# Kernel optimization log

Measured on AMD Instinct MI355X. Metric: run time of the kernel, lower is better.

Reference implementation:

```python
import jax, jax.numpy as jnp
import numpy as np

H, CH, PQ, PV = 12, 16, 4, 8
C_S = 384
INF, EPS = 1e5, 1e-8
PT_W = -0.5


def setup_inputs() -> dict:
    key = jax.random.key(0)
    ks = jax.random.split(key, 20)
    B, C, N = 1, 8, 256
    s = jax.random.normal(ks[0], (B, C, N, C_S), jnp.float32)
    z = jax.random.normal(ks[1], (B, C, N, N, 8), jnp.float32)
    A = jax.random.normal(ks[2], (B, C, N, 3, 3), jnp.float32)
    rot = jnp.linalg.qr(A)[0]  # proper orthonormal frames
    trans = jax.random.normal(ks[3], (B, C, N, 3), jnp.float32) * 10.0
    mask = jnp.ones((B, C, N), jnp.float32)
    w = lambda k, i, o: jax.random.normal(k, (i, o), jnp.float32) * 0.02
    hc = H * CH
    return {
        's': s, 'z': z, 'rot': rot, 'trans': trans, 'mask': mask,
        'wq': w(ks[4], C_S, hc), 'bq': jnp.zeros((hc,)),
        'wkv': w(ks[5], C_S, 2 * hc), 'bkv': jnp.zeros((2 * hc,)),
        'g_gamma': jnp.ones((C_S,)), 'g_beta': jnp.zeros((C_S,)),
        'wgq': w(ks[6], C_S, hc), 'bgq': jnp.zeros((hc,)),
        'wgk': w(ks[7], C_S, hc), 'bgk': jnp.zeros((hc,)),
        'wqp': w(ks[8], C_S, H * PQ * 3), 'bqp': jnp.zeros((H * PQ * 3,)),
        'wkvp': w(ks[9], C_S, H * (PQ + PV) * 3), 'bkvp': jnp.zeros((H * (PQ + PV) * 3,)),
        'head_weights': jnp.full((H,), 0.5413248538970947, jnp.float32),  # softplus^-1(1)
        'wdist': w(ks[10], 1, H), 'bdist': jnp.zeros((H,)),
        'wout': w(ks[11], H * (CH + 4 * PV), C_S), 'bout': jnp.zeros((C_S,)),
    }


def _forward(s, z, rot, trans, mask, wq, bq, wkv, bkv, g_gamma, g_beta,
             wgq, bgq, wgk, bgk, wqp, bqp, wkvp, bkvp, head_weights,
             wdist, bdist, wout, bout):
    B, C, N, _ = s.shape
    q = (s @ wq + bq).reshape(B, C, N, H, CH)
    kv = (s @ wkv + bkv).reshape(B, C, N, H, 2 * CH)
    k, v = kv[..., :CH], kv[..., CH:]
    scale = (1.0 / (3 * CH)) ** 0.5
    a = jnp.einsum('bcihd,bcjhd->bchij', q, k) * scale  # [B,C,H,N,N]
    # global feature: mean over conformations, LayerNorm, QK bias
    s_g = s.mean(axis=-3)
    mu = s_g.mean(-1, keepdims=True)
    var = ((s_g - mu) ** 2).mean(-1, keepdims=True)
    s_gn = (s_g - mu) / jnp.sqrt(var + 1e-5) * g_gamma + g_beta
    g_q = (s_gn @ wgq + bgq).reshape(B, N, H, CH)
    g_k = (s_gn @ wgk + bgk).reshape(B, N, H, CH)
    a = a + jnp.einsum('bihd,bjhd->bhij', g_q, g_k)[:, None] * scale
    # invariant point attention term
    def to_pts(raw, P):
        pts = jnp.stack(jnp.split(raw, 3, axis=-1), axis=-1)  # [B,C,N,H*P,3]
        pts = jnp.einsum('bcnij,bcnpj->bcnpi', rot, pts) + trans[..., None, :]
        return pts.reshape(B, C, N, H, P, 3)
    q_pts = to_pts(s @ wqp + bqp, PQ)
    kv_pts = to_pts(s @ wkvp + bkvp, PQ + PV)
    k_pts, v_pts = kv_pts[..., :PQ, :], kv_pts[..., PQ:, :]
    diff2 = jnp.sum((q_pts[:, :, :, None] - k_pts[:, :, None]) ** 2, axis=-1)  # [B,C,N,N,H,PQ]
    hw = jax.nn.softplus(head_weights) * (1.0 / (3 * (PQ * 9.0 / 2))) ** 0.5
    pt_att = jnp.sum(diff2 * hw[:, None], axis=-1) * PT_W  # [B,C,N,N,H]
    a = a + jnp.moveaxis(pt_att, -1, -3)
    # mask
    sq_mask = mask[..., :, None] * mask[..., None, :]
    a = a + (INF * (sq_mask - 1.0))[..., None, :, :]
    # distance bias (torch uses a raw .view -> reshape, not transpose)
    dist = jnp.sqrt(jnp.sum((trans[..., :, None, :] - trans[..., None, :, :]) ** 2, axis=-1))
    db = dist[..., None] * wdist[0] + bdist  # [B,C,N,N,H]
    a = a + db.reshape(B, C, H, N, N)
    a = jax.nn.softmax(a, axis=-1)
    o = jnp.einsum('bchij,bcjhd->bcihd', a, v).reshape(B, C, N, H * CH)
    o_pt = jnp.einsum('bchij,bcjhpd->bcihpd', a, v_pts)  # [B,C,N,H,PV,3]
    o_pt = jnp.einsum('bcnji,bcnhpj->bcnhpi', rot, o_pt - trans[:, :, :, None, None, :])
    o_pt_norm = jnp.sqrt(jnp.sum(o_pt ** 2, axis=-1) + EPS).reshape(B, C, N, H * PV)
    o_pt_f = o_pt.reshape(B, C, N, H * PV, 3)
    feat = jnp.concatenate([o, o_pt_f[..., 0], o_pt_f[..., 1], o_pt_f[..., 2], o_pt_norm], axis=-1)
    return feat @ wout + bout, a


def reference(s, z, rot, trans, mask, wq, bq, wkv, bkv, g_gamma, g_beta,
              wgq, bgq, wgk, bgk, wqp, bqp, wkvp, bkvp, head_weights,
              wdist, bdist, wout, bout):
    return _forward(s, z, rot, trans, mask, wq, bq, wkv, bkv, g_gamma, g_beta,
                    wgq, bgq, wgk, bgk, wqp, bqp, wkvp, bkvp, head_weights,
                    wdist, bdist, wout, bout)
```

## Files before the change

### kernel.cpp

```cpp
#include <hip/hip_runtime.h>
#include <math.h>

#define NRES 256
#define CDIM 8
#define HNUM 12
#define CS   384

typedef __attribute__((ext_vector_type(8))) short bf16x8;
typedef __attribute__((ext_vector_type(4))) float f32x4;
typedef unsigned short ushort_t;

static __device__ __forceinline__ unsigned short f2bf(float x) {
    unsigned int u = __float_as_uint(x);
    unsigned int r = (u + 0x7fffu + ((u >> 16) & 1u)) >> 16;
    return (unsigned short)r;
}
static __device__ __forceinline__ float bf2f(unsigned short h) {
    return __uint_as_float(((unsigned int)h) << 16);
}

__global__ __launch_bounds__(256) void convert_kernel(
    const float* __restrict__ s,
    const float* __restrict__ wq, const float* __restrict__ bq,
    const float* __restrict__ wkv, const float* __restrict__ bkv,
    const float* __restrict__ wqp, const float* __restrict__ bqp,
    const float* __restrict__ wkvp, const float* __restrict__ bkvp,
    const float* __restrict__ wgq, const float* __restrict__ bgq,
    const float* __restrict__ wgk, const float* __restrict__ bgk,
    const float* __restrict__ wout,
    ushort_t* __restrict__ s_bf, ushort_t* __restrict__ wt_bf,
    ushort_t* __restrict__ wtg_bf, float* __restrict__ pbias,
    float* __restrict__ gbias,
    ushort_t* __restrict__ wo_hi, ushort_t* __restrict__ wo_lo)
{
    const int idx = blockIdx.x*256 + threadIdx.x;
    const int NS   = 2048*384;
    const int NWT  = 384*1152;
    const int NWTG = 384*384;
    const int NWO  = 576*384;
    if (idx < NS) {
        s_bf[idx] = f2bf(s[idx]);
    } else if (idx < NS + NWT) {
        const int t = idx - NS;
        const int k = t / 1152, vc = t - k*1152;
        const float* w; int C, lc;
        if (vc < 192)      { w = wq;   C = 192; lc = vc; }
        else if (vc < 576) { w = wkv;  C = 384; lc = vc - 192; }
        else if (vc < 720) { w = wqp;  C = 144; lc = vc - 576; }
        else               { w = wkvp; C = 432; lc = vc - 720; }
        wt_bf[(size_t)vc*384 + k] = f2bf(w[(size_t)k*C + lc]);
    } else if (idx < NS + NWT + NWTG) {
        const int t = idx - NS - NWT;
        const int k = t / 384, vc = t - k*384;
        const float val = (vc < 192) ? wgq[(size_t)k*192 + vc]
                                     : wgk[(size_t)k*192 + vc - 192];
        wtg_bf[(size_t)vc*384 + k] = f2bf(val);
    } else if (idx < NS + NWT + NWTG + 1152) {
        const int i = idx - NS - NWT - NWTG;
        float b;
        if (i < 192)      b = bq[i];
        else if (i < 576) b = bkv[i - 192];
        else if (i < 720) b = bqp[i - 576];
        else              b = bkvp[i - 720];
        pbias[i] = b;
    } else if (idx < NS + NWT + NWTG + 1152 + 384) {
        const int i = idx - NS - NWT - NWTG - 1152;
        gbias[i] = (i < 192) ? bgq[i] : bgk[i - 192];
    } else if (idx < NS + NWT + NWTG + 1536 + NWO) {
        const int t = idx - NS - NWT - NWTG - 1536;
        const int k = t / 384, n = t - k*384;
        const float wv = wout[t];
        const unsigned int u = __float_as_uint(wv);
        const float hif = __uint_as_float(u & 0xFFFF0000u);
        wo_hi[(size_t)n*576 + k] = (ushort_t)(u >> 16);
        wo_lo[(size_t)n*576 + k] = (ushort_t)(__float_as_uint(wv - hif) >> 16);
    }
}

__global__ __launch_bounds__(256) void proj_mfma_kernel(
    const ushort_t* __restrict__ s_bf, const ushort_t* __restrict__ wt_bf,
    const float* __restrict__ pbias,
    float* __restrict__ qo, float* __restrict__ ko, float* __restrict__ vo,
    float* __restrict__ rawp)
{
    const int blk = blockIdx.x;
    const int rt = blk / 18, ct = blk - rt*18;
    const int r0 = rt * 64, c0 = ct * 64;
    const int tid = threadIdx.x;
    const int wave = tid >> 6, lane = tid & 63;
    const int wrow = wave >> 1, wcol = wave & 1;
    const int m0 = r0 + wrow*32, n0 = c0 + wcol*32;
    const int qd = lane >> 4, lr = lane & 15;

    f32x4 acc00 = {0,0,0,0}, acc01 = {0,0,0,0}, acc10 = {0,0,0,0}, acc11 = {0,0,0,0};

    const ushort_t* a0p = s_bf  + (size_t)(m0 + lr)*384 + qd*8;
    const ushort_t* a1p = a0p + 16*384;
    const ushort_t* b0p = wt_bf + (size_t)(n0 + lr)*384 + qd*8;
    const ushort_t* b1p = b0p + 16*384;

    #pragma unroll
    for (int kk = 0; kk < 384; kk += 32) {
        const bf16x8 a0 = *(const bf16x8*)(a0p + kk);
        const bf16x8 a1 = *(const bf16x8*)(a1p + kk);
        const bf16x8 b0 = *(const bf16x8*)(b0p + kk);
        const bf16x8 b1 = *(const bf16x8*)(b1p + kk);
        acc00 = __builtin_amdgcn_mfma_f32_16x16x32_bf16(a0, b0, acc00, 0, 0, 0);
        acc01 = __builtin_amdgcn_mfma_f32_16x16x32_bf16(a0, b1, acc01, 0, 0, 0);
        acc10 = __builtin_amdgcn_mfma_f32_16x16x32_bf16(a1, b0, acc10, 0, 0, 0);
        acc11 = __builtin_amdgcn_mfma_f32_16x16x32_bf16(a1, b1, acc11, 0, 0, 0);
    }

    #pragma unroll
    for (int mt = 0; mt < 2; ++mt) {
        #pragma unroll
        for (int nt = 0; nt < 2; ++nt) {
            const f32x4 av = (mt==0) ? (nt==0 ? acc00 : acc01)
                                     : (nt==0 ? acc10 : acc11);
            const int col = n0 + nt*16 + lr;
            const float bb = pbias[col];
            #pragma unroll
            for (int reg = 0; reg < 4; ++reg) {
                const int row = m0 + mt*16 + qd*4 + reg;
                const float val = av[reg] + bb;
                if (col < 192) {
                    qo[(size_t)row*192 + col] = val;
                } else if (col < 576) {
                    const int lc = col - 192, h = lc >> 5, rm = lc & 31;
                    if (rm < 16) ko[(size_t)row*192 + h*16 + rm] = val;
                    else         vo[(size_t)row*192 + h*16 + rm - 16] = val;
                } else {
                    rawp[(size_t)row*576 + col - 576] = val;
                }
            }
        }
    }
}

__global__ __launch_bounds__(256) void pt_transform_kernel(
    const float* __restrict__ rawp, const float* __restrict__ rot,
    const float* __restrict__ trans,
    float* __restrict__ qpo, float* __restrict__ kpo, float* __restrict__ vpo)
{
    const int t = blockIdx.x*256 + threadIdx.x;
    const int row = t / 192;
    const int p = t - row*192;
    const float* R = rot + (size_t)row*9;
    const float* T = trans + (size_t)row*3;
    const float* base = rawp + (size_t)row*576;
    float x, y, z;
    if (p < 48) { x = base[p];       y = base[48+p];  z = base[96+p]; }
    else { const int pk = p-48; x = base[144+pk]; y = base[288+pk]; z = base[432+pk]; }
    const float px = R[0]*x + R[1]*y + R[2]*z + T[0];
    const float py = R[3]*x + R[4]*y + R[5]*z + T[1];
    const float pz = R[6]*x + R[7]*y + R[8]*z + T[2];
    if (p < 48) {
        float* o = qpo + (size_t)row*144 + p*3;
        o[0]=px; o[1]=py; o[2]=pz;
    } else {
        const int pk = p-48, h = pk/12, pp = pk - h*12;
        if (pp < 4) { float* o = kpo + (size_t)row*144 + (h*4+pp)*3;     o[0]=px; o[1]=py; o[2]=pz; }
        else        { float* o = vpo + (size_t)row*288 + (h*8+(pp-4))*3; o[0]=px; o[1]=py; o[2]=pz; }
    }
}

__global__ __launch_bounds__(256) void ln_kernel(
    const float* __restrict__ s, const float* __restrict__ g_gamma,
    const float* __restrict__ g_beta, ushort_t* __restrict__ sgn_bf)
{
    const int n = blockIdx.x;
    const int tid = threadIdx.x;
    __shared__ float sg[CS];
    __shared__ float red[256];

    for (int d = tid; d < CS; d += 256) {
        float acc = 0.f;
        for (int c = 0; c < CDIM; ++c) acc += s[((size_t)c*NRES+n)*CS + d];
        sg[d] = acc * (1.0f/CDIM);
    }
    __syncthreads();

    float lsum = 0.f;
    for (int d = tid; d < CS; d += 256) lsum += sg[d];
    red[tid] = lsum; __syncthreads();
    for (int st = 128; st > 0; st >>= 1) { if (tid < st) red[tid] += red[tid+st]; __syncthreads(); }
    const float mean = red[0] * (1.0f/CS);
    __syncthreads();

    float lvar = 0.f;
    for (int d = tid; d < CS; d += 256) { float df = sg[d]-mean; lvar += df*df; }
    red[tid] = lvar; __syncthreads();
    for (int st = 128; st > 0; st >>= 1) { if (tid < st) red[tid] += red[tid+st]; __syncthreads(); }
    const float var = red[0] * (1.0f/CS);
    __syncthreads();

    const float inv = rsqrtf(var + 1e-5f);
    for (int d = tid; d < CS; d += 256)
        sgn_bf[(size_t)n*CS + d] = f2bf((sg[d]-mean)*inv*g_gamma[d] + g_beta[d]);
}

__global__ __launch_bounds__(256) void ggemm_mfma_kernel(
    const ushort_t* __restrict__ sgn_bf, const ushort_t* __restrict__ wtg_bf,
    const float* __restrict__ gbias,
    float* __restrict__ gqo, float* __restrict__ gko)
{
    const int blk = blockIdx.x;
    const int rt = blk / 6, ct = blk - rt*6;
    const int r0 = rt * 64, c0 = ct * 64;
    const int tid = threadIdx.x;
    const int wave = tid >> 6, lane = tid & 63;
    const int wrow = wave >> 1, wcol = wave & 1;
    const int m0 = r0 + wrow*32, n0 = c0 + wcol*32;
    const int qd = lane >> 4, lr = lane & 15;

    f32x4 acc00 = {0,0,0,0}, acc01 = {0,0,0,0}, acc10 = {0,0,0,0}, acc11 = {0,0,0,0};

    const ushort_t* a0p = sgn_bf + (size_t)(m0 + lr)*384 + qd*8;
    const ushort_t* a1p = a0p + 16*384;
    const ushort_t* b0p = wtg_bf + (size_t)(n0 + lr)*384 + qd*8;
    const ushort_t* b1p = b0p + 16*384;

    #pragma unroll
    for (int kk = 0; kk < 384; kk += 32) {
        const bf16x8 a0 = *(const bf16x8*)(a0p + kk);
        const bf16x8 a1 = *(const bf16x8*)(a1p + kk);
        const bf16x8 b0 = *(const bf16x8*)(b0p + kk);
        const bf16x8 b1 = *(const bf16x8*)(b1p + kk);
        acc00 = __builtin_amdgcn_mfma_f32_16x16x32_bf16(a0, b0, acc00, 0, 0, 0);
        acc01 = __builtin_amdgcn_mfma_f32_16x16x32_bf16(a0, b1, acc01, 0, 0, 0);
        acc10 = __builtin_amdgcn_mfma_f32_16x16x32_bf16(a1, b0, acc10, 0, 0, 0);
        acc11 = __builtin_amdgcn_mfma_f32_16x16x32_bf16(a1, b1, acc11, 0, 0, 0);
    }

    #pragma unroll
    for (int mt = 0; mt < 2; ++mt) {
        #pragma unroll
        for (int nt = 0; nt < 2; ++nt) {
            const f32x4 av = (mt==0) ? (nt==0 ? acc00 : acc01)
                                     : (nt==0 ? acc10 : acc11);
            const int col = n0 + nt*16 + lr;
            const float bb = gbias[col];
            #pragma unroll
            for (int reg = 0; reg < 4; ++reg) {
                const int row = m0 + mt*16 + qd*4 + reg;
                const float val = av[reg] + bb;
                if (col < 192) gqo[(size_t)row*192 + col]       = val;
                else           gko[(size_t)row*192 + col - 192] = val;
            }
        }
    }
}

#define BSTR 104
__global__ __launch_bounds__(256) void attn_mfma_kernel(
    const float* __restrict__ q, const float* __restrict__ k,
    const float* __restrict__ q_pts, const float* __restrict__ k_pts,
    const float* __restrict__ g_q, const float* __restrict__ g_k,
    const float* __restrict__ trans, const float* __restrict__ mask,
    const float* __restrict__ head_weights, const float* __restrict__ wdist,
    const float* __restrict__ bdist, float* __restrict__ a_out)
{
    const int blk  = blockIdx.x;
    const int qtr  = blk & 3;
    const int ch   = blk >> 2;
    const int h    = ch % HNUM;
    const int c    = ch / HNUM;
    const int i0   = qtr * 64;
    const int tid  = threadIdx.x;

    __shared__ ushort_t Bsh[256*BSTR];
    __shared__ ushort_t Ash[64*BSTR];
    __shared__ float dsh[7*256];
    __shared__ float msh[256];
    __shared__ float kn_sh[256];
    __shared__ float qn_sh[64];
    __shared__ float wdsh[12], bdsh[12];
    __shared__ float cpart[96];
    __shared__ float censh[3];

    msh[tid] = mask[c*NRES + tid];
    if (tid < 12) { wdsh[tid] = wdist[tid]; bdsh[tid] = bdist[tid]; }

    if (tid < 96) {
        const int coord = tid % 3, chunk = tid / 3;
        float sv = 0.f;
        for (int e = 0; e < 8; ++e)
            sv += trans[((size_t)c*NRES + chunk*8 + e)*3 + coord];
        cpart[tid] = sv;
    }
    __syncthreads();
    if (tid < 3) {
        float sv = 0.f;
        for (int e = 0; e < 32; ++e) sv += cpart[e*3 + tid];
        censh[tid] = sv * (1.0f/256.0f);
    }
    __syncthreads();

    const float s54   = 0.13608276348795434f;
    const float scale = 0.14433756729740643f;
    const float hwv = 0.5f * logf(1.0f + expf(head_weights[h])) * s54;
    const float sh  = sqrtf(2.0f * hwv);
    const float cx = censh[0], cy = censh[1], cz = censh[2];
    const float cen3[3] = {cx, cy, cz};

    {
        const int j = tid;
        const float4* kr4 = (const float4*)(k    + ((size_t)c*NRES + j)*192 + h*16);
        const float4* gk4 = (const float4*)(g_k  + (size_t)j*192 + h*16);
        const float4* kp4 = (const float4*)(k_pts+ ((size_t)c*NRES + j)*144 + h*12);
        ushort_t* br = &Bsh[j*BSTR];
        #pragma unroll
        for (int e4 = 0; e4 < 4; ++e4) {
            const float4 w = kr4[e4];
            br[e4*4+0] = f2bf(w.x); br[e4*4+1] = f2bf(w.y);
            br[e4*4+2] = f2bf(w.z); br[e4*4+3] = f2bf(w.w);
        }
        #pragma unroll
        for (int e4 = 0; e4 < 4; ++e4) {
            const float4 w = gk4[e4];
            br[16+e4*4+0] = f2bf(w.x); br[16+e4*4+1] = f2bf(w.y);
            br[16+e4*4+2] = f2bf(w.z); br[16+e4*4+3] = f2bf(w.w);
        }
        float kp_a[12];
        #pragma unroll
        for (int e4 = 0; e4 < 3; ++e4) {
            const float4 w = kp4[e4];
            kp_a[e4*4+0]=w.x; kp_a[e4*4+1]=w.y; kp_a[e4*4+2]=w.z; kp_a[e4*4+3]=w.w;
        }
        float kn = 0.f;
        #pragma unroll
        for (int e = 0; e < 12; ++e) {
            const float kp = kp_a[e] - cen3[e % 3];
            kn += kp*kp;
            const float sp = sh * kp;
            const unsigned int u = __float_as_uint(sp);
            const float hif = __uint_as_float(u & 0xFFFF0000u);
            const ushort_t hi = (ushort_t)(u >> 16);
            br[32+e] = hi;
            br[44+e] = (ushort_t)(__float_as_uint(sp - hif) >> 16);
            br[56+e] = hi;
        }
        #pragma unroll
        for (int e = 68; e < 96; ++e) br[e] = 0;
        kn_sh[j] = hwv * kn;
    }

    if (tid < 64) {
        const int il = i0 + tid;
        const float4* qr4 = (const float4*)(q    + ((size_t)c*NRES + il)*192 + h*16);
        const float4* gq4 = (const float4*)(g_q  + (size_t)il*192 + h*16);
        const float4* qp4 = (const float4*)(q_pts+ ((size_t)c*NRES + il)*144 + h*12);
        ushort_t* ar = &Ash[tid*BSTR];
        #pragma unroll
        for (int e4 = 0; e4 < 4; ++e4) {
            const float4 w = qr4[e4];
            ar[e4*4+0] = f2bf(scale*w.x); ar[e4*4+1] = f2bf(scale*w.y);
            ar[e4*4+2] = f2bf(scale*w.z); ar[e4*4+3] = f2bf(scale*w.w);
        }
        #pragma unroll
        for (int e4 = 0; e4 < 4; ++e4) {
            const float4 w = gq4[e4];
            ar[16+e4*4+0] = f2bf(scale*w.x); ar[16+e4*4+1] = f2bf(scale*w.y);
            ar[16+e4*4+2] = f2bf(scale*w.z); ar[16+e4*4+3] = f2bf(scale*w.w);
        }
        float qp_a[12];
        #pragma unroll
        for (int e4 = 0; e4 < 3; ++e4) {
            const float4 w = qp4[e4];
            qp_a[e4*4+0]=w.x; qp_a[e4*4+1]=w.y; qp_a[e4*4+2]=w.z; qp_a[e4*4+3]=w.w;
        }
        float qn = 0.f;
        #pragma unroll
        for (int e = 0; e < 12; ++e) {
            const float qp = qp_a[e] - cen3[e % 3];
            qn += qp*qp;
            const float sp = sh * qp;
            const unsigned int u = __float_as_uint(sp);
            const float hif = __uint_as_float(u & 0xFFFF0000u);
            const ushort_t hi = (ushort_t)(u >> 16);
            ar[32+e] = hi;
            ar[44+e] = hi;
            ar[56+e] = (ushort_t)(__float_as_uint(sp - hif) >> 16);
        }
        #pragma unroll
        for (int e = 68; e < 96; ++e) ar[e] = 0;
        qn_sh[tid] = hwv * qn;
    }

    const int Fmin = h*65536 + i0*256;
    const int iibase = Fmin / 3072;
    const int NI = (Fmin + 63*256 + 255)/3072 - iibase + 1;
    const float* tch = trans + (size_t)c*768;
    for (int idx = tid; idx < NI*256; idx += 256) {
        const int e = idx >> 8, jj = idx & 255;
        const int ia = iibase + e;
        const float dx = tch[ia*3+0] - tch[jj*3+0];
        const float dy = tch[ia*3+1] - tch[jj*3+1];
        const float dz = tch[ia*3+2] - tch[jj*3+2];
        dsh[idx] = sqrtf(dx*dx + dy*dy + dz*dz);
    }
    __syncthreads();

    const int wave = tid >> 6, lane = tid & 63;
    const int qd = lane >> 4, lr = lane & 15;
    const int m0 = wave*16;

    const ushort_t* ap = &Ash[(m0 + lr)*BSTR + qd*8];
    const bf16x8 af0 = *(const bf16x8*)(ap);
    const bf16x8 af1 = *(const bf16x8*)(ap + 32);
    const bf16x8 af2 = *(const bf16x8*)(ap + 64);

    f32x4 acc[16];
    #pragma unroll
    for (int t = 0; t < 16; ++t) {
        const ushort_t* bp = &Bsh[(t*16 + lr)*BSTR + qd*8];
        f32x4 a = {0.f,0.f,0.f,0.f};
        a = __builtin_amdgcn_mfma_f32_16x16x32_bf16(af0, *(const bf16x8*)(bp),      a, 0, 0, 0);
        a = __builtin_amdgcn_mfma_f32_16x16x32_bf16(af1, *(const bf16x8*)(bp + 32), a, 0, 0, 0);
        a = __builtin_amdgcn_mfma_f32_16x16x32_bf16(af2, *(const bf16x8*)(bp + 64), a, 0, 0, 0);
        acc[t] = a;
    }

    const int ibase = m0 + qd*4;
    float qn_r[4], mb_r[4];
    int F0_[4];
    #pragma unroll
    for (int r = 0; r < 4; ++r) {
        const int il = i0 + ibase + r;
        qn_r[r] = qn_sh[ibase + r];
        mb_r[r] = 100000.0f * msh[il];
        F0_[r]  = h*65536 + il*256;
    }

    float mx[4] = {-1e30f,-1e30f,-1e30f,-1e30f};
    #pragma unroll
// ... 1 lines not shown
        const int j = t*16 + lr;
        const float knj = kn_sh[j];
        const float mj  = msh[j];
        #pragma unroll
        for (int r = 0; r < 4; ++r) {
            const unsigned int f = (unsigned int)(F0_[r] + j);
            const unsigned int p = f / 12u;
            const int ho = (int)(f - p*12u);
            const int ii = (int)(p >> 8);
            const int jj = (int)(p & 255u);
            const float dist = dsh[(ii - iibase)*256 + jj];
            const float db = dist*wdsh[ho] + bdsh[ho];
            const float lv = acc[t][r] - qn_r[r] - knj
                           + (mb_r[r]*mj - 100000.0f) + db;
            acc[t][r] = lv;
            mx[r] = fmaxf(mx[r], lv);
        }
    }
    #pragma unroll
    for (int r = 0; r < 4; ++r) {
        #pragma unroll
        for (int off = 1; off < 16; off <<= 1)
            mx[r] = fmaxf(mx[r], __shfl_xor(mx[r], off));
    }
    float sm[4] = {0.f,0.f,0.f,0.f};
    #pragma unroll
    for (int t = 0; t < 16; ++t) {
        #pragma unroll
        for (int r = 0; r < 4; ++r) {
            const float e = __expf(acc[t][r] - mx[r]);
            acc[t][r] = e;
            sm[r] += e;
        }
    }
    #pragma unroll
    for (int r = 0; r < 4; ++r) {
        #pragma unroll
        for (int off = 1; off < 16; off <<= 1)
            sm[r] += __shfl_xor(sm[r], off);
        sm[r] = 1.0f / sm[r];
    }
    float* dst = a_out + ((size_t)ch*NRES + (i0 + ibase))*NRES;
    #pragma unroll
    for (int t = 0; t < 16; ++t) {
        #pragma unroll
        for (int r = 0; r < 4; ++r)
            dst[(size_t)r*NRES + t*16 + lr] = acc[t][r]*sm[r];
    }
}

#define ASTRB 264
__global__ __launch_bounds__(256) void out_feat_mfma_kernel(
    const float* __restrict__ a, const float* __restrict__ v,
    const float* __restrict__ v_pts, const float* __restrict__ rot,
    const float* __restrict__ trans,
    ushort_t* __restrict__ feat_hi, ushort_t* __restrict__ feat_lo)
{
    const int blk = blockIdx.x;
    const int qtr = blk & 3;
    const int ch  = blk >> 2;
    const int h   = ch % HNUM;
    const int c   = ch / HNUM;
    const int i0  = qtr * 64;
    const int tid = threadIdx.x;

    __shared__ ushort_t Bt[64*ASTRB];
    __shared__ float opt[64*25];
    __shared__ float osh[64*17];
    __shared__ float cpart[96];
    __shared__ float censh[3];

    if (tid < 96) {
        const int coord = tid % 3, chunk = tid / 3;
        float sv = 0.f;
        for (int e = 0; e < 8; ++e)
            sv += trans[((size_t)c*NRES + chunk*8 + e)*3 + coord];
        cpart[tid] = sv;
    }
    __syncthreads();
    if (tid < 3) {
        float sv = 0.f;
        for (int e = 0; e < 32; ++e) sv += cpart[e*3 + tid];
        censh[tid] = sv * (1.0f/256.0f);
    }
    __syncthreads();
    const float cx = censh[0], cy = censh[1], cz = censh[2];
    const float cen3[3] = {cx, cy, cz};

    {
        const int j = tid;
        const float4* vr = (const float4*)(v + ((size_t)c*NRES + j)*192 + h*16);
        #pragma unroll
        for (int e4 = 0; e4 < 4; ++e4) {
            const float4 w = vr[e4];
            Bt[(e4*4+0)*ASTRB + j] = f2bf(w.x);
            Bt[(e4*4+1)*ASTRB + j] = f2bf(w.y);
            Bt[(e4*4+2)*ASTRB + j] = f2bf(w.z);
            Bt[(e4*4+3)*ASTRB + j] = f2bf(w.w);
        }
        const float4* vpr = (const float4*)(v_pts + ((size_t)c*NRES + j)*288 + h*24);
        #pragma unroll
        for (int e4 = 0; e4 < 6; ++e4) {
            const float4 w = vpr[e4];
            const float vals[4] = {w.x, w.y, w.z, w.w};
            #pragma unroll
            for (int cc = 0; cc < 4; ++cc) {
                const int e = e4*4 + cc;
                const float vp = vals[cc] - cen3[e % 3];
                const unsigned int u = __float_as_uint(vp);
                const float hif = __uint_as_float(u & 0xFFFF0000u);
                Bt[(16+e)*ASTRB + j] = (ushort_t)(u >> 16);
                Bt[(40+e)*ASTRB + j] = (ushort_t)(__float_as_uint(vp - hif) >> 16);
            }
        }
    }
    __syncthreads();

    const int wave = tid >> 6, lane = tid & 63;
    const int qd = lane >> 4, lr = lane & 15;
    const int m0 = wave*16;

    const float* arow = a + ((size_t)ch*NRES + i0 + m0 + lr)*NRES;

    f32x4 acc[4] = {{0,0,0,0},{0,0,0,0},{0,0,0,0},{0,0,0,0}};
    #pragma unroll
    for (int kk = 0; kk < 256; kk += 32) {
        const float4 a0 = *(const float4*)(arow + qd*8 + kk);
        const float4 a1 = *(const float4*)(arow + qd*8 + kk + 4);
        const float av[8] = {a0.x,a0.y,a0.z,a0.w,a1.x,a1.y,a1.z,a1.w};
        bf16x8 ahi, alo;
        #pragma unroll
        for (int e = 0; e < 8; ++e) {
            const unsigned int u = __float_as_uint(av[e]);
            const float hif = __uint_as_float(u & 0xFFFF0000u);
            ((ushort_t*)&ahi)[e] = (ushort_t)(u >> 16);
            ((ushort_t*)&alo)[e] = (ushort_t)(__float_as_uint(av[e] - hif) >> 16);
        }
        #pragma unroll
        for (int t = 0; t < 4; ++t) {
            const bf16x8 bf = *(const bf16x8*)&Bt[(t*16 + lr)*ASTRB + qd*8 + kk];
            acc[t] = __builtin_amdgcn_mfma_f32_16x16x32_bf16(ahi, bf, acc[t], 0, 0, 0);
            acc[t] = __builtin_amdgcn_mfma_f32_16x16x32_bf16(alo, bf, acc[t], 0, 0, 0);
        }
    }

    #pragma unroll
    for (int reg = 0; reg < 4; ++reg) {
        const int row_l = m0 + qd*4 + reg;
        osh[row_l*17 + lr] = acc[0][reg];
        opt[row_l*25 + lr] = acc[1][reg];
    }
    #pragma unroll
    for (int reg = 0; reg < 4; ++reg) {
        const int row_l = m0 + qd*4 + reg;
        if (lr < 8) opt[row_l*25 + 16 + lr] = acc[2][reg];
        else        opt[row_l*25 + (lr-8)] += acc[2][reg];
    }
    #pragma unroll
    for (int reg = 0; reg < 4; ++reg) {
        const int row_l = m0 + qd*4 + reg;
        opt[row_l*25 + 8 + lr] += acc[3][reg];
// ... 81 lines not shown
        acc[1][0] = __builtin_amdgcn_mfma_f32_16x16x32_bf16(fl1, wh0, acc[1][0], 0, 0, 0);
        acc[1][1] = __builtin_amdgcn_mfma_f32_16x16x32_bf16(fl1, wh1, acc[1][1], 0, 0, 0);
        acc[0][0] = __builtin_amdgcn_mfma_f32_16x16x32_bf16(fh0, wl0, acc[0][0], 0, 0, 0);
        acc[0][1] = __builtin_amdgcn_mfma_f32_16x16x32_bf16(fh0, wl1, acc[0][1], 0, 0, 0);
        acc[1][0] = __builtin_amdgcn_mfma_f32_16x16x32_bf16(fh1, wl0, acc[1][0], 0, 0, 0);
        acc[1][1] = __builtin_amdgcn_mfma_f32_16x16x32_bf16(fh1, wl1, acc[1][1], 0, 0, 0);
    }

    #pragma unroll
    for (int mt = 0; mt < 2; ++mt) {
        #pragma unroll
        for (int nt = 0; nt < 2; ++nt) {
            const int col = n0 + nt*16 + lr;
            const float bb = bout[col];
            #pragma unroll
            for (int reg = 0; reg < 4; ++reg) {
                const int row = m0 + mt*16 + qd*4 + reg;
                out0[(size_t)row*CS + col] = acc[mt][nt][reg] + bb;
            }
        }
    }
}

extern "C" void kernel_launch(void* const* d_in, const int* in_sizes, int n_in,
                              void* d_out, int out_size, void* d_ws, size_t ws_size,
                              hipStream_t stream)
{
    const float* s     = (const float*)d_in[0];
    const float* rot   = (const float*)d_in[2];
    const float* trans = (const float*)d_in[3];
    const float* mask  = (const float*)d_in[4];
    const float* wq    = (const float*)d_in[5];
    const float* bq    = (const float*)d_in[6];
    const float* wkv   = (const float*)d_in[7];
    const float* bkv   = (const float*)d_in[8];
    const float* g_gamma = (const float*)d_in[9];
    const float* g_beta  = (const float*)d_in[10];
    const float* wgq   = (const float*)d_in[11];
    const float* bgq   = (const float*)d_in[12];
    const float* wgk   = (const float*)d_in[13];
    const float* bgk   = (const float*)d_in[14];
    const float* wqp   = (const float*)d_in[15];
    const float* bqp   = (const float*)d_in[16];
    const float* wkvp  = (const float*)d_in[17];
    const float* bkvp  = (const float*)d_in[18];
    const float* head_weights = (const float*)d_in[19];
    const float* wdist = (const float*)d_in[20];
    const float* bdist = (const float*)d_in[21];
    const float* wout  = (const float*)d_in[22];
    const float* bout  = (const float*)d_in[23];

    float* ws      = (float*)d_ws;
    float* q_buf   = ws + 0;
    float* qp_buf  = ws + 393216;
    float* kp_buf  = ws + 688128;
    float* gq_buf  = ws + 983040;
    float* gk_buf  = ws + 1032192;
    float* k_buf   = ws + 1081344;
    float* v_buf   = ws + 1474560;
    float* vp_buf  = ws + 1867776;
    ushort_t* sgn_bf  = (ushort_t*)(ws + 1867776);
    ushort_t* feat_hi = (ushort_t*)(ws + 2457600);
    ushort_t* feat_lo = (ushort_t*)(ws + 3047424);
    ushort_t* wo_hi   = (ushort_t*)(ws + 3637248);
    ushort_t* wo_lo   = (ushort_t*)(ws + 3747840);

    float* out0  = (float*)d_out;
    float* a_out = out0 + 786432;
    float*    rawp   = a_out;
    ushort_t* s_bf   = (ushort_t*)(a_out + 1179648);
    ushort_t* wt_bf  = (ushort_t*)(a_out + 1572864);
    ushort_t* wtg_bf = (ushort_t*)(a_out + 1794048);
    float*    pbias  = a_out + 1867776;
    float*    gbias  = a_out + 1868928;

    convert_kernel<<<6246, 256, 0, stream>>>(s, wq, bq, wkv, bkv, wqp, bqp,
                                             wkvp, bkvp, wgq, bgq, wgk, bgk, wout,
                                             s_bf, wt_bf, wtg_bf, pbias, gbias,
                                             wo_hi, wo_lo);
    ln_kernel<<<256, 256, 0, stream>>>(s, g_gamma, g_beta, sgn_bf);
    proj_mfma_kernel<<<576, 256, 0, stream>>>(s_bf, wt_bf, pbias,
                                              q_buf, k_buf, v_buf, rawp);
    ggemm_mfma_kernel<<<24, 256, 0, stream>>>(sgn_bf, wtg_bf, gbias,
                                              gq_buf, gk_buf);
    pt_transform_kernel<<<1536, 256, 0, stream>>>(rawp, rot, trans,
                                                  qp_buf, kp_buf, vp_buf);
    attn_mfma_kernel<<<384, 256, 0, stream>>>(q_buf, k_buf, qp_buf, kp_buf,
                                              gq_buf, gk_buf, trans, mask,
                                              head_weights, wdist, bdist, a_out);
    out_feat_mfma_kernel<<<384, 256, 0, stream>>>(a_out, v_buf, vp_buf, rot, trans,
                                                  feat_hi, feat_lo);
    out_gemm_mfma_kernel<<<192, 256, 0, stream>>>(feat_hi, feat_lo, wo_hi, wo_lo,
                                                  bout, out0);
}
```

Before: 211.9 us.

## Merge prep kernels and fold point transform into attention and output kernels

Three launch-level fusions cut the pipeline from eight kernels to five. The weight conversion and LayerNorm kernels become one launch, and the projection GEMM and global-feature GEMM share another, dispatched by block index. The separate point-transform kernel is removed: the attention and output-feature kernels now read the raw projected points and apply the rotation and translation themselves. This drops two launches and a full write and read of the transformed point buffers, at the cost of redoing the frame transform in each consuming block and moving rawp into the workspace.

```diff
diff --git a/kernel.cpp b/kernel.cpp
--- a/kernel.cpp
+++ b/kernel.cpp
@@ -15,11 +15,8 @@
     unsigned int r = (u + 0x7fffu + ((u >> 16) & 1u)) >> 16;
     return (unsigned short)r;
 }
-static __device__ __forceinline__ float bf2f(unsigned short h) {
-    return __uint_as_float(((unsigned int)h) << 16);
-}
-
-__global__ __launch_bounds__(256) void convert_kernel(
+
+__global__ __launch_bounds__(256) void convert_ln_kernel(
     const float* __restrict__ s,
     const float* __restrict__ wq, const float* __restrict__ bq,
     const float* __restrict__ wkv, const float* __restrict__ bkv,
@@ -28,151 +25,65 @@
     const float* __restrict__ wgq, const float* __restrict__ bgq,
     const float* __restrict__ wgk, const float* __restrict__ bgk,
     const float* __restrict__ wout,
+    const float* __restrict__ g_gamma, const float* __restrict__ g_beta,
     ushort_t* __restrict__ s_bf, ushort_t* __restrict__ wt_bf,
     ushort_t* __restrict__ wtg_bf, float* __restrict__ pbias,
     float* __restrict__ gbias,
-    ushort_t* __restrict__ wo_hi, ushort_t* __restrict__ wo_lo)
+    ushort_t* __restrict__ wo_hi, ushort_t* __restrict__ wo_lo,
+    ushort_t* __restrict__ sgn_bf)
 {
-    const int idx = blockIdx.x*256 + threadIdx.x;
+    __shared__ float sg[CS];
+    __shared__ float red[256];
+    const int tid = threadIdx.x;
     const int NS   = 2048*384;
     const int NWT  = 384*1152;
     const int NWTG = 384*384;
     const int NWO  = 576*384;
-    if (idx < NS) {
-        s_bf[idx] = f2bf(s[idx]);
-    } else if (idx < NS + NWT) {
-        const int t = idx - NS;
-        const int k = t / 1152, vc = t - k*1152;
-        const float* w; int C, lc;
-        if (vc < 192)      { w = wq;   C = 192; lc = vc; }
-        else if (vc < 576) { w = wkv;  C = 384; lc = vc - 192; }
-        else if (vc < 720) { w = wqp;  C = 144; lc = vc - 576; }
-        else               { w = wkvp; C = 432; lc = vc - 720; }
-        wt_bf[(size_t)vc*384 + k] = f2bf(w[(size_t)k*C + lc]);
-    } else if (idx < NS + NWT + NWTG) {
-        const int t = idx - NS - NWT;
-        const int k = t / 384, vc = t - k*384;
-        const float val = (vc < 192) ? wgq[(size_t)k*192 + vc]
-                                     : wgk[(size_t)k*192 + vc - 192];
-        wtg_bf[(size_t)vc*384 + k] = f2bf(val);
-    } else if (idx < NS + NWT + NWTG + 1152) {
-        const int i = idx - NS - NWT - NWTG;
-        float b;
-        if (i < 192)      b = bq[i];
-        else if (i < 576) b = bkv[i - 192];
-        else if (i < 720) b = bqp[i - 576];
-        else              b = bkvp[i - 720];
-        pbias[i] = b;
-    } else if (idx < NS + NWT + NWTG + 1152 + 384) {
-        const int i = idx - NS - NWT - NWTG - 1152;
-        gbias[i] = (i < 192) ? bgq[i] : bgk[i - 192];
-    } else if (idx < NS + NWT + NWTG + 1536 + NWO) {
-        const int t = idx - NS - NWT - NWTG - 1536;
-        const int k = t / 384, n = t - k*384;
-        const float wv = wout[t];
-        const unsigned int u = __float_as_uint(wv);
-        const float hif = __uint_as_float(u & 0xFFFF0000u);
-        wo_hi[(size_t)n*576 + k] = (ushort_t)(u >> 16);
-        wo_lo[(size_t)n*576 + k] = (ushort_t)(__float_as_uint(wv - hif) >> 16);
-    }
-}
-
-__global__ __launch_bounds__(256) void proj_mfma_kernel(
-    const ushort_t* __restrict__ s_bf, const ushort_t* __restrict__ wt_bf,
-    const float* __restrict__ pbias,
-    float* __restrict__ qo, float* __restrict__ ko, float* __restrict__ vo,
-    float* __restrict__ rawp)
-{
-    const int blk = blockIdx.x;
-    const int rt = blk / 18, ct = blk - rt*18;
-    const int r0 = rt * 64, c0 = ct * 64;
-    const int tid = threadIdx.x;
-    const int wave = tid >> 6, lane = tid & 63;
-    const int wrow = wave >> 1, wcol = wave & 1;
-    const int m0 = r0 + wrow*32, n0 = c0 + wcol*32;
-    const int qd = lane >> 4, lr = lane & 15;
-
-    f32x4 acc00 = {0,0,0,0}, acc01 = {0,0,0,0}, acc10 = {0,0,0,0}, acc11 = {0,0,0,0};
-
-    const ushort_t* a0p = s_bf  + (size_t)(m0 + lr)*384 + qd*8;
-    const ushort_t* a1p = a0p + 16*384;
-    const ushort_t* b0p = wt_bf + (size_t)(n0 + lr)*384 + qd*8;
-    const ushort_t* b1p = b0p + 16*384;
-
-    #pragma unroll
-    for (int kk = 0; kk < 384; kk += 32) {
-        const bf16x8 a0 = *(const bf16x8*)(a0p + kk);
-        const bf16x8 a1 = *(const bf16x8*)(a1p + kk);
-        const bf16x8 b0 = *(const bf16x8*)(b0p + kk);
-        const bf16x8 b1 = *(const bf16x8*)(b1p + kk);
-        acc00 = __builtin_amdgcn_mfma_f32_16x16x32_bf16(a0, b0, acc00, 0, 0, 0);
-        acc01 = __builtin_amdgcn_mfma_f32_16x16x32_bf16(a0, b1, acc01, 0, 0, 0);
-        acc10 = __builtin_amdgcn_mfma_f32_16x16x32_bf16(a1, b0, acc10, 0, 0, 0);
-        acc11 = __builtin_amdgcn_mfma_f32_16x16x32_bf16(a1, b1, acc11, 0, 0, 0);
-    }
-
-    #pragma unroll
-    for (int mt = 0; mt < 2; ++mt) {
-        #pragma unroll
-        for (int nt = 0; nt < 2; ++nt) {
-            const f32x4 av = (mt==0) ? (nt==0 ? acc00 : acc01)
-                                     : (nt==0 ? acc10 : acc11);
-            const int col = n0 + nt*16 + lr;
-            const float bb = pbias[col];
-            #pragma unroll
-            for (int reg = 0; reg < 4; ++reg) {
-                const int row = m0 + mt*16 + qd*4 + reg;
-                const float val = av[reg] + bb;
-                if (col < 192) {
-                    qo[(size_t)row*192 + col] = val;
-                } else if (col < 576) {
-                    const int lc = col - 192, h = lc >> 5, rm = lc & 31;
-                    if (rm < 16) ko[(size_t)row*192 + h*16 + rm] = val;
-                    else         vo[(size_t)row*192 + h*16 + rm - 16] = val;
-                } else {
-                    rawp[(size_t)row*576 + col - 576] = val;
-                }
-            }
-        }
-    }
-}
-
-__global__ __launch_bounds__(256) void pt_transform_kernel(
-    const float* __restrict__ rawp, const float* __restrict__ rot,
-    const float* __restrict__ trans,
-    float* __restrict__ qpo, float* __restrict__ kpo, float* __restrict__ vpo)
-{
-    const int t = blockIdx.x*256 + threadIdx.x;
-    const int row = t / 192;
-    const int p = t - row*192;
-    const float* R = rot + (size_t)row*9;
-    const float* T = trans + (size_t)row*3;
-    const float* base = rawp + (size_t)row*576;
-    float x, y, z;
-    if (p < 48) { x = base[p];       y = base[48+p];  z = base[96+p]; }
-    else { const int pk = p-48; x = base[144+pk]; y = base[288+pk]; z = base[432+pk]; }
-    const float px = R[0]*x + R[1]*y + R[2]*z + T[0];
-    const float py = R[3]*x + R[4]*y + R[5]*z + T[1];
-    const float pz = R[6]*x + R[7]*y + R[8]*z + T[2];
-    if (p < 48) {
-        float* o = qpo + (size_t)row*144 + p*3;
-        o[0]=px; o[1]=py; o[2]=pz;
-    } else {
-        const int pk = p-48, h = pk/12, pp = pk - h*12;
-        if (pp < 4) { float* o = kpo + (size_t)row*144 + (h*4+pp)*3;     o[0]=px; o[1]=py; o[2]=pz; }
-        else        { float* o = vpo + (size_t)row*288 + (h*8+(pp-4))*3; o[0]=px; o[1]=py; o[2]=pz; }
-    }
-}
-
-__global__ __launch_bounds__(256) void ln_kernel(
-    const float* __restrict__ s, const float* __restrict__ g_gamma,
-    const float* __restrict__ g_beta, ushort_t* __restrict__ sgn_bf)
-{
-    const int n = blockIdx.x;
-    const int tid = threadIdx.x;
-    __shared__ float sg[CS];
-    __shared__ float red[256];
-
+    const int NB_CONV = 6246;
+
+    if (blockIdx.x < NB_CONV) {
+        const int idx = blockIdx.x*256 + tid;
+        if (idx < NS) {
+            s_bf[idx] = f2bf(s[idx]);
+        } else if (idx < NS + NWT) {
+            const int t = idx - NS;
+            const int k = t / 1152, vc = t - k*1152;
+            const float* w; int C, lc;
+            if (vc < 192)      { w = wq;   C = 192; lc = vc; }
+            else if (vc < 576) { w = wkv;  C = 384; lc = vc - 192; }
+            else if (vc < 720) { w = wqp;  C = 144; lc = vc - 576; }
+            else               { w = wkvp; C = 432; lc = vc - 720; }
+            wt_bf[(size_t)vc*384 + k] = f2bf(w[(size_t)k*C + lc]);
+        } else if (idx < NS + NWT + NWTG) {
+            const int t = idx - NS - NWT;
+            const int k = t / 384, vc = t - k*384;
+            const float val = (vc < 192) ? wgq[(size_t)k*192 + vc]
+                                         : wgk[(size_t)k*192 + vc - 192];
+            wtg_bf[(size_t)vc*384 + k] = f2bf(val);
+        } else if (idx < NS + NWT + NWTG + 1152) {
+            const int i = idx - NS - NWT - NWTG;
+            float b;
+            if (i < 192)      b = bq[i];
+            else if (i < 576) b = bkv[i - 192];
+            else if (i < 720) b = bqp[i - 576];
+            else              b = bkvp[i - 720];
+            pbias[i] = b;
+        } else if (idx < NS + NWT + NWTG + 1152 + 384) {
+            const int i = idx - NS - NWT - NWTG - 1152;
+            gbias[i] = (i < 192) ? bgq[i] : bgk[i - 192];
+        } else if (idx < NS + NWT + NWTG + 1536 + NWO) {
+            const int t = idx - NS - NWT - NWTG - 1536;
+            const int k = t / 384, n = t - k*384;
+            const float wv = wout[t];
+            const unsigned int u = __float_as_uint(wv);
+            const float hif = __uint_as_float(u & 0xFFFF0000u);
+            wo_hi[(size_t)n*576 + k] = (ushort_t)(u >> 16);
+            wo_lo[(size_t)n*576 + k] = (ushort_t)(__float_as_uint(wv - hif) >> 16);
+        }
+        return;
+    }
+
+    const int n = blockIdx.x - NB_CONV;
     for (int d = tid; d < CS; d += 256) {
         float acc = 0.f;
         for (int c = 0; c < CDIM; ++c) acc += s[((size_t)c*NRES+n)*CS + d];
@@ -199,19 +110,75 @@
         sgn_bf[(size_t)n*CS + d] = f2bf((sg[d]-mean)*inv*g_gamma[d] + g_beta[d]);
 }
 
-__global__ __launch_bounds__(256) void ggemm_mfma_kernel(
+__global__ __launch_bounds__(256) void proj_ggemm_kernel(
+    const ushort_t* __restrict__ s_bf, const ushort_t* __restrict__ wt_bf,
+    const float* __restrict__ pbias,
     const ushort_t* __restrict__ sgn_bf, const ushort_t* __restrict__ wtg_bf,
     const float* __restrict__ gbias,
-    float* __restrict__ gqo, float* __restrict__ gko)
+    float* __restrict__ qo, float* __restrict__ ko, float* __restrict__ vo,
+    float* __restrict__ rawp, float* __restrict__ gqo, float* __restrict__ gko)
 {
-    const int blk = blockIdx.x;
-    const int rt = blk / 6, ct = blk - rt*6;
-    const int r0 = rt * 64, c0 = ct * 64;
     const int tid = threadIdx.x;
     const int wave = tid >> 6, lane = tid & 63;
     const int wrow = wave >> 1, wcol = wave & 1;
+    const int qd = lane >> 4, lr = lane & 15;
+
+    if (blockIdx.x < 576) {
+        const int blk = blockIdx.x;
+        const int rt = blk / 18, ct = blk - rt*18;
+        const int r0 = rt * 64, c0 = ct * 64;
+        const int m0 = r0 + wrow*32, n0 = c0 + wcol*32;
+
+        f32x4 acc00 = {0,0,0,0}, acc01 = {0,0,0,0}, acc10 = {0,0,0,0}, acc11 = {0,0,0,0};
+
+        const ushort_t* a0p = s_bf  + (size_t)(m0 + lr)*384 + qd*8;
+        const ushort_t* a1p = a0p + 16*384;
+        const ushort_t* b0p = wt_bf + (size_t)(n0 + lr)*384 + qd*8;
+        const ushort_t* b1p = b0p + 16*384;
+
+        #pragma unroll
+        for (int kk = 0; kk < 384; kk += 32) {
+            const bf16x8 a0 = *(const bf16x8*)(a0p + kk);
+            const bf16x8 a1 = *(const bf16x8*)(a1p + kk);
+            const bf16x8 b0 = *(const bf16x8*)(b0p + kk);
+            const bf16x8 b1 = *(const bf16x8*)(b1p + kk);
+            acc00 = __builtin_amdgcn_mfma_f32_16x16x32_bf16(a0, b0, acc00, 0, 0, 0);
+            acc01 = __builtin_amdgcn_mfma_f32_16x16x32_bf16(a0, b1, acc01, 0, 0, 0);
+            acc10 = __builtin_amdgcn_mfma_f32_16x16x32_bf16(a1, b0, acc10, 0, 0, 0);
+            acc11 = __builtin_amdgcn_mfma_f32_16x16x32_bf16(a1, b1, acc11, 0, 0, 0);
+        }
+
+        #pragma unroll
+        for (int mt = 0; mt < 2; ++mt) {
+            #pragma unroll
+            for (int nt = 0; nt < 2; ++nt) {
+                const f32x4 av = (mt==0) ? (nt==0 ? acc00 : acc01)
+                                         : (nt==0 ? acc10 : acc11);
+                const int col = n0 + nt*16 + lr;
+                const float bb = pbias[col];
+                #pragma unroll
+                for (int reg = 0; reg < 4; ++reg) {
+                    const int row = m0 + mt*16 + qd*4 + reg;
+                    const float val = av[reg] + bb;
+                    if (col < 192) {
+                        qo[(size_t)row*192 + col] = val;
+                    } else if (col < 576) {
+                        const int lc = col - 192, h = lc >> 5, rm = lc & 31;
+                        if (rm < 16) ko[(size_t)row*192 + h*16 + rm] = val;
+                        else         vo[(size_t)row*192 + h*16 + rm - 16] = val;
+                    } else {
+                        rawp[(size_t)row*576 + col - 576] = val;
+                    }
+                }
+            }
+        }
+        return;
+    }
+
+    const int blk = blockIdx.x - 576;
+    const int rt = blk / 6, ct = blk - rt*6;
+    const int r0 = rt * 64, c0 = ct * 64;
     const int m0 = r0 + wrow*32, n0 = c0 + wcol*32;
-    const int qd = lane >> 4, lr = lane & 15;
 
     f32x4 acc00 = {0,0,0,0}, acc01 = {0,0,0,0}, acc10 = {0,0,0,0}, acc11 = {0,0,0,0};
 
@@ -254,7 +221,7 @@
 #define BSTR 104
 __global__ __launch_bounds__(256) void attn_mfma_kernel(
     const float* __restrict__ q, const float* __restrict__ k,
-    const float* __restrict__ q_pts, const float* __restrict__ k_pts,
+    const float* __restrict__ rawp, const float* __restrict__ rot,
     const float* __restrict__ g_q, const float* __restrict__ g_k,
     const float* __restrict__ trans, const float* __restrict__ mask,
     const float* __restrict__ head_weights, const float* __restrict__ wdist,
@@ -301,13 +268,12 @@
     const float hwv = 0.5f * logf(1.0f + expf(head_weights[h])) * s54;
     const float sh  = sqrtf(2.0f * hwv);
     const float cx = censh[0], cy = censh[1], cz = censh[2];
-    const float cen3[3] = {cx, cy, cz};
 
     {
         const int j = tid;
-        const float4* kr4 = (const float4*)(k    + ((size_t)c*NRES + j)*192 + h*16);
-        const float4* gk4 = (const float4*)(g_k  + (size_t)j*192 + h*16);
-        const float4* kp4 = (const float4*)(k_pts+ ((size_t)c*NRES + j)*144 + h*12);
+        const int grow = c*NRES + j;
+        const float4* kr4 = (const float4*)(k   + (size_t)grow*192 + h*16);
+        const float4* gk4 = (const float4*)(g_k + (size_t)j*192 + h*16);
         ushort_t* br = &Bsh[j*BSTR];
         #pragma unroll
         for (int e4 = 0; e4 < 4; ++e4) {
@@ -321,24 +287,36 @@
             br[16+e4*4+0] = f2bf(w.x); br[16+e4*4+1] = f2bf(w.y);
             br[16+e4*4+2] = f2bf(w.z); br[16+e4*4+3] = f2bf(w.w);
         }
-        float kp_a[12];
-        #pragma unroll
-        for (int e4 = 0; e4 < 3; ++e4) {
-            const float4 w = kp4[e4];
-            kp_a[e4*4+0]=w.x; kp_a[e4*4+1]=w.y; kp_a[e4*4+2]=w.z; kp_a[e4*4+3]=w.w;
-        }
+        const float* base = rawp + (size_t)grow*576;
+        const float4 rx = *(const float4*)(base + 144 + h*12);
+        const float4 ry = *(const float4*)(base + 288 + h*12);
+        const float4 rz = *(const float4*)(base + 432 + h*12);
+        const float* R = rot + (size_t)grow*9;
+        const float* T = trans + (size_t)grow*3;
+        const float R0=R[0],R1=R[1],R2=R[2],R3=R[3],R4=R[4],R5=R[5],R6=R[6],R7=R[7],R8=R[8];
+        const float Tx=T[0]-cx, Ty=T[1]-cy, Tz=T[2]-cz;
+        const float xs[4] = {rx.x, rx.y, rx.z, rx.w};
+        const float ys[4] = {ry.x, ry.y, ry.z, ry.w};
+        const float zs[4] = {rz.x, rz.y, rz.z, rz.w};
         float kn = 0.f;
         #pragma unroll
-        for (int e = 0; e < 12; ++e) {
-            const float kp = kp_a[e] - cen3[e % 3];
-            kn += kp*kp;
-            const float sp = sh * kp;
-            const unsigned int u = __float_as_uint(sp);
-            const float hif = __uint_as_float(u & 0xFFFF0000u);
-            const ushort_t hi = (ushort_t)(u >> 16);
-            br[32+e] = hi;
-            br[44+e] = (ushort_t)(__float_as_uint(sp - hif) >> 16);
-            br[56+e] = hi;
+        for (int pp = 0; pp < 4; ++pp) {
+            const float x = xs[pp], y = ys[pp], z = zs[pp];
+            const float pv[3] = { R0*x + R1*y + R2*z + Tx,
+                                  R3*x + R4*y + R5*z + Ty,
+                                  R6*x + R7*y + R8*z + Tz };
+            #pragma unroll
+            for (int cc = 0; cc < 3; ++cc) {
+                const int e = pp*3 + cc;
+                kn += pv[cc]*pv[cc];
+                const float sp = sh * pv[cc];
+                const unsigned int u = __float_as_uint(sp);
+                const float hif = __uint_as_float(u & 0xFFFF0000u);
+                const ushort_t hi = (ushort_t)(u >> 16);
+                br[32+e] = hi;
+                br[44+e] = (ushort_t)(__float_as_uint(sp - hif) >> 16);
+                br[56+e] = hi;
+            }
         }
         #pragma unroll
         for (int e = 68; e < 96; ++e) br[e] = 0;
@@ -347,9 +325,9 @@
 
     if (tid < 64) {
         const int il = i0 + tid;
-        const float4* qr4 = (const float4*)(q    + ((size_t)c*NRES + il)*192 + h*16);
-        const float4* gq4 = (const float4*)(g_q  + (size_t)il*192 + h*16);
-        const float4* qp4 = (const float4*)(q_pts+ ((size_t)c*NRES + il)*144 + h*12);
+        const int grow = c*NRES + il;
+        const float4* qr4 = (const float4*)(q   + (size_t)grow*192 + h*16);
+        const float4* gq4 = (const float4*)(g_q + (size_t)il*192 + h*16);
         ushort_t* ar = &Ash[tid*BSTR];
         #pragma unroll
         for (int e4 = 0; e4 < 4; ++e4) {
@@ -363,24 +341,36 @@
             ar[16+e4*4+0] = f2bf(scale*w.x); ar[16+e4*4+1] = f2bf(scale*w.y);
             ar[16+e4*4+2] = f2bf(scale*w.z); ar[16+e4*4+3] = f2bf(scale*w.w);
         }
-        float qp_a[12];
-        #pragma unroll
-        for (int e4 = 0; e4 < 3; ++e4) {
-            const float4 w = qp4[e4];
-            qp_a[e4*4+0]=w.x; qp_a[e4*4+1]=w.y; qp_a[e4*4+2]=w.z; qp_a[e4*4+3]=w.w;
-        }
+        const float* base = rawp + (size_t)grow*576;
+        const float4 rx = *(const float4*)(base + h*4);
+        const float4 ry = *(const float4*)(base + 48 + h*4);
+        const float4 rz = *(const float4*)(base + 96 + h*4);
+        const float* R = rot + (size_t)grow*9;
+        const float* T = trans + (size_t)grow*3;
+        const float R0=R[0],R1=R[1],R2=R[2],R3=R[3],R4=R[4],R5=R[5],R6=R[6],R7=R[7],R8=R[8];
+        const float Tx=T[0]-cx, Ty=T[1]-cy, Tz=T[2]-cz;
+        const float xs[4] = {rx.x, rx.y, rx.z, rx.w};
+        const float ys[4] = {ry.x, ry.y, ry.z, ry.w};
+        const float zs[4] = {rz.x, rz.y, rz.z, rz.w};
         float qn = 0.f;
         #pragma unroll
-        for (int e = 0; e < 12; ++e) {
-            const float qp = qp_a[e] - cen3[e % 3];
-            qn += qp*qp;
-            const float sp = sh * qp;
-            const unsigned int u = __float_as_uint(sp);
-            const float hif = __uint_as_float(u & 0xFFFF0000u);
-            const ushort_t hi = (ushort_t)(u >> 16);
-            ar[32+e] = hi;
-            ar[44+e] = hi;
-            ar[56+e] = (ushort_t)(__float_as_uint(sp - hif) >> 16);
+        for (int pp = 0; pp < 4; ++pp) {
+            const float x = xs[pp], y = ys[pp], z = zs[pp];
+            const float pv[3] = { R0*x + R1*y + R2*z + Tx,
+                                  R3*x + R4*y + R5*z + Ty,
+                                  R6*x + R7*y + R8*z + Tz };
+            #pragma unroll
+            for (int cc = 0; cc < 3; ++cc) {
+                const int e = pp*3 + cc;
+                qn += pv[cc]*pv[cc];
+                const float sp = sh * pv[cc];
+                const unsigned int u = __float_as_uint(sp);
+                const float hif = __uint_as_float(u & 0xFFFF0000u);
+                const ushort_t hi = (ushort_t)(u >> 16);
+                ar[32+e] = hi;
+                ar[44+e] = hi;
+                ar[56+e] = (ushort_t)(__float_as_uint(sp - hif) >> 16);
+            }
         }
         #pragma unroll
         for (int e = 68; e < 96; ++e) ar[e] = 0;
@@ -488,7 +478,7 @@
 #define ASTRB 264
 __global__ __launch_bounds__(256) void out_feat_mfma_kernel(
     const float* __restrict__ a, const float* __restrict__ v,
-    const float* __restrict__ v_pts, const float* __restrict__ rot,
+    const float* __restrict__ rawp, const float* __restrict__ rot,
     const float* __restrict__ trans,
     ushort_t* __restrict__ feat_hi, ushort_t* __restrict__ feat_lo)
 {
@@ -521,11 +511,11 @@
     }
     __syncthreads();
     const float cx = censh[0], cy = censh[1], cz = censh[2];
-    const float cen3[3] = {cx, cy, cz};
 
     {
         const int j = tid;
-        const float4* vr = (const float4*)(v + ((size_t)c*NRES + j)*192 + h*16);
+        const int grow = c*NRES + j;
+        const float4* vr = (const float4*)(v + (size_t)grow*192 + h*16);
         #pragma unroll
         for (int e4 = 0; e4 < 4; ++e4) {
             const float4 w = vr[e4];
@@ -534,15 +524,30 @@
             Bt[(e4*4+2)*ASTRB + j] = f2bf(w.z);
             Bt[(e4*4+3)*ASTRB + j] = f2bf(w.w);
         }
-        const float4* vpr = (const float4*)(v_pts + ((size_t)c*NRES + j)*288 + h*24);
-        #pragma unroll
-        for (int e4 = 0; e4 < 6; ++e4) {
-            const float4 w = vpr[e4];
-            const float vals[4] = {w.x, w.y, w.z, w.w};
+        const float* base = rawp + (size_t)grow*576;
+        const float4 rx0 = *(const float4*)(base + 144 + h*12 + 4);
+        const float4 rx1 = *(const float4*)(base + 144 + h*12 + 8);
+        const float4 ry0 = *(const float4*)(base + 288 + h*12 + 4);
+        const float4 ry1 = *(const float4*)(base + 288 + h*12 + 8);
+        const float4 rz0 = *(const float4*)(base + 432 + h*12 + 4);
+        const float4 rz1 = *(const float4*)(base + 432 + h*12 + 8);
+        const float* R = rot + (size_t)grow*9;
+        const float* T = trans + (size_t)grow*3;
+        const float R0=R[0],R1=R[1],R2=R[2],R3=R[3],R4=R[4],R5=R[5],R6=R[6],R7=R[7],R8=R[8];
+        const float Tx=T[0]-cx, Ty=T[1]-cy, Tz=T[2]-cz;
+        const float xs[8] = {rx0.x,rx0.y,rx0.z,rx0.w, rx1.x,rx1.y,rx1.z,rx1.w};
+        const float ys[8] = {ry0.x,ry0.y,ry0.z,ry0.w, ry1.x,ry1.y,ry1.z,ry1.w};
+        const float zs[8] = {rz0.x,rz0.y,rz0.z,rz0.w, rz1.x,rz1.y,rz1.z,rz1.w};
+        #pragma unroll
+        for (int pp = 0; pp < 8; ++pp) {
+            const float x = xs[pp], y = ys[pp], z = zs[pp];
+            const float pv[3] = { R0*x + R1*y + R2*z + Tx,
+                                  R3*x + R4*y + R5*z + Ty,
+                                  R6*x + R7*y + R8*z + Tz };
             #pragma unroll
-            for (int cc = 0; cc < 4; ++cc) {
-                const int e = e4*4 + cc;
-                const float vp = vals[cc] - cen3[e % 3];
+            for (int cc = 0; cc < 3; ++cc) {
+                const int e = pp*3 + cc;
+                const float vp = pv[cc];
                 const unsigned int u = __float_as_uint(vp);
                 const float hif = __uint_as_float(u & 0xFFFF0000u);
                 Bt[(16+e)*ASTRB + j] = (ushort_t)(u >> 16);
@@ -730,43 +735,38 @@
 
     float* ws      = (float*)d_ws;
     float* q_buf   = ws + 0;
-    float* qp_buf  = ws + 393216;
-    float* kp_buf  = ws + 688128;
     float* gq_buf  = ws + 983040;
     float* gk_buf  = ws + 1032192;
     float* k_buf   = ws + 1081344;
     float* v_buf   = ws + 1474560;
-    float* vp_buf  = ws + 1867776;
     ushort_t* sgn_bf  = (ushort_t*)(ws + 1867776);
     ushort_t* feat_hi = (ushort_t*)(ws + 2457600);
     ushort_t* feat_lo = (ushort_t*)(ws + 3047424);
     ushort_t* wo_hi   = (ushort_t*)(ws + 3637248);
     ushort_t* wo_lo   = (ushort_t*)(ws + 3747840);
+    float*    rawp    = ws + 4194304;
 
     float* out0  = (float*)d_out;
     float* a_out = out0 + 786432;
-    float*    rawp   = a_out;
-    ushort_t* s_bf   = (ushort_t*)(a_out + 1179648);
-    ushort_t* wt_bf  = (ushort_t*)(a_out + 1572864);
-    ushort_t* wtg_bf = (ushort_t*)(a_out + 1794048);
-    float*    pbias  = a_out + 1867776;
-    float*    gbias  = a_out + 1868928;
-
-    convert_kernel<<<6246, 256, 0, stream>>>(s, wq, bq, wkv, bkv, wqp, bqp,
-                                             wkvp, bkvp, wgq, bgq, wgk, bgk, wout,
-                                             s_bf, wt_bf, wtg_bf, pbias, gbias,
-                                             wo_hi, wo_lo);
-    ln_kernel<<<256, 256, 0, stream>>>(s, g_gamma, g_beta, sgn_bf);
-    proj_mfma_kernel<<<576, 256, 0, stream>>>(s_bf, wt_bf, pbias,
-                                              q_buf, k_buf, v_buf, rawp);
-    ggemm_mfma_kernel<<<24, 256, 0, stream>>>(sgn_bf, wtg_bf, gbias,
-                                              gq_buf, gk_buf);
-    pt_transform_kernel<<<1536, 256, 0, stream>>>(rawp, rot, trans,
-                                                  qp_buf, kp_buf, vp_buf);
-    attn_mfma_kernel<<<384, 256, 0, stream>>>(q_buf, k_buf, qp_buf, kp_buf,
+    ushort_t* s_bf   = (ushort_t*)(a_out);
+    ushort_t* wt_bf  = (ushort_t*)(a_out + 393216);
+    ushort_t* wtg_bf = (ushort_t*)(a_out + 614400);
+    float*    pbias  = a_out + 688128;
+    float*    gbias  = a_out + 689280;
+
+    convert_ln_kernel<<<6502, 256, 0, stream>>>(s, wq, bq, wkv, bkv, wqp, bqp,
+                                                wkvp, bkvp, wgq, bgq, wgk, bgk,
+                                                wout, g_gamma, g_beta,
+                                                s_bf, wt_bf, wtg_bf, pbias, gbias,
+                                                wo_hi, wo_lo, sgn_bf);
+    proj_ggemm_kernel<<<600, 256, 0, stream>>>(s_bf, wt_bf, pbias,
+                                               sgn_bf, wtg_bf, gbias,
+                                               q_buf, k_buf, v_buf, rawp,
+                                               gq_buf, gk_buf);
+    attn_mfma_kernel<<<384, 256, 0, stream>>>(q_buf, k_buf, rawp, rot,
                                               gq_buf, gk_buf, trans, mask,
                                               head_weights, wdist, bdist, a_out);
-    out_feat_mfma_kernel<<<384, 256, 0, stream>>>(a_out, v_buf, vp_buf, rot, trans,
+    out_feat_mfma_kernel<<<384, 256, 0, stream>>>(a_out, v_buf, rawp, rot, trans,
                                                   feat_hi, feat_lo);
     out_gemm_mfma_kernel<<<192, 256, 0, stream>>>(feat_hi, feat_lo, wo_hi, wo_lo,
                                                   bout, out0);
```

Result: faster. 200.4 us (-5.4%).
